# Kernel tuning notes

Hardware: AMD Instinct MI355X
Metric: run time of the kernel (lower is better)

The kernel has to match this reference:

```python
import jax, jax.numpy as jnp
import numpy as np

B, C, H, W = 8, 256, 128, 128
K = 7
DILS = (1, 2, 3)
HIDDEN = C // 16
EPS = 1e-5


def _bn(y, g, b, m, v):
    # eval-mode BatchNorm1d on (B,C,L)
    return (y - m[None, :, None]) * (g * jax.lax.rsqrt(v + EPS))[None, :, None] + b[None, :, None]


def _dw_conv1d(s, w, dil):
    # depthwise dilated Conv1d; s: (B,C,L), w: (C,1,K) torch layout == OIH
    pad = dil * (w.shape[-1] - 1) // 2
    return jax.lax.conv_general_dilated(
        s, w, window_strides=(1,), padding=[(pad, pad)],
        rhs_dilation=(dil,), dimension_numbers=('NCH', 'OIH', 'NCH'),
        feature_group_count=s.shape[1])


def _dir_weight(xp, sq_w, sq_b, convs, bn_g, bn_b, bn_m, bn_v):
    # xp: (B, L_ortho, C, L) -> weight (B, C, L)
    pmax = jnp.max(xp, axis=1)            # (B,C,L)
    pavg = jnp.mean(xp, axis=1)           # (B,C,L)
    # 1x1 Conv2d(2->1) == scalar mix of the two pooled maps
    s = sq_w[0] * pmax + sq_w[1] * pavg + sq_b
    y = _dw_conv1d(s, convs[0], DILS[0])
    for i in range(1, len(DILS)):
        y = y + _dw_conv1d(s, convs[i], DILS[i])
    return jax.nn.sigmoid(_bn(y, bn_g, bn_b, bn_m, bn_v))


def setup_inputs() -> dict:
    key = jax.random.key(0)
    ks = jax.random.split(key, 24)
    def n(k, shape, scale=0.1):
        return jax.random.normal(k, shape, dtype=jnp.float32) * scale
    return {
        "x": jax.random.normal(ks[0], (B, C, H, W), dtype=jnp.float32),
        "hw_sq_w": n(ks[1], (2,), 0.5), "hw_sq_b": n(ks[2], (1,), 0.1),
        "hw_conv": n(ks[3], (len(DILS), C, 1, K)),
        "hw_bn_g": 1.0 + n(ks[4], (C,)), "hw_bn_b": n(ks[5], (C,)),
        "hw_bn_m": n(ks[6], (C,)), "hw_bn_v": 1.0 + 0.1 * jax.random.uniform(ks[7], (C,)),
        "ww_sq_w": n(ks[8], (2,), 0.5), "ww_sq_b": n(ks[9], (1,), 0.1),
        "ww_conv": n(ks[10], (len(DILS), C, 1, K)),
        "ww_bn_g": 1.0 + n(ks[11], (C,)), "ww_bn_b": n(ks[12], (C,)),
        "ww_bn_m": n(ks[13], (C,)), "ww_bn_v": 1.0 + 0.1 * jax.random.uniform(ks[14], (C,)),
        "gate_w": 1.0 + n(ks[15], (C,)),
        "gate_bn_g": 1.0 + n(ks[16], (C,)), "gate_bn_b": n(ks[17], (C,)),
        "gate_bn_m": n(ks[18], (C,)), "gate_bn_v": 1.0 + 0.1 * jax.random.uniform(ks[19], (C,)),
        "mix_W": n(ks[20], (2, 2), 0.5), "mix_b": n(ks[21], (2,), 0.1),
        "ca_fc1": n(ks[22], (HIDDEN, C)), "ca_fc2": n(ks[23], (C, HIDDEN)),
        "alpha": jnp.float32(1.0), "beta": jnp.float32(1.0),
    }


def reference(x, hw_sq_w, hw_sq_b, hw_conv, hw_bn_g, hw_bn_b, hw_bn_m, hw_bn_v,
              ww_sq_w, ww_sq_b, ww_conv, ww_bn_g, ww_bn_b, ww_bn_m, ww_bn_v,
              gate_w, gate_bn_g, gate_bn_b, gate_bn_m, gate_bn_v,
              mix_W, mix_b, ca_fc1, ca_fc2, alpha, beta):
    b, c, h, w = x.shape
    # height-direction weight: pool over W, strip conv over H
    x_h_in = jnp.transpose(x, (0, 3, 1, 2))                                  # (B,W,C,H)
    w_h = _dir_weight(x_h_in, hw_sq_w, hw_sq_b, hw_conv, hw_bn_g, hw_bn_b, hw_bn_m, hw_bn_v)  # (B,C,H)
    x_h_out = jnp.transpose(x_h_in * w_h[:, None], (0, 2, 3, 1))             # (B,C,H,W)
    # width-direction weight: pool over H, strip conv over W
    x_w_in = jnp.transpose(x, (0, 2, 1, 3))                                  # (B,H,C,W)
    w_w = _dir_weight(x_w_in, ww_sq_w, ww_sq_b, ww_conv, ww_bn_g, ww_bn_b, ww_bn_m, ww_bn_v)  # (B,C,W)
    x_w_out = jnp.transpose(x_w_in * w_w[:, None], (0, 2, 1, 3))             # (B,C,H,W)

    # orientation mix (gate_fc is SHARED between directions)
    def gate(seq):  # (B,C,L) -> (B,C)
        y = jax.nn.relu(_bn(seq * gate_w[None, :, None], gate_bn_g, gate_bn_b, gate_bn_m, gate_bn_v))
        return jnp.mean(y, axis=-1)

    g = jnp.stack([gate(w_h), gate(w_w)], axis=-1)                           # (B,C,2)
    lam = jax.nn.softmax(g @ mix_W.T + mix_b, axis=-1)
    lam_h = lam[..., 0][:, :, None, None]
    lam_w = lam[..., 1][:, :, None, None]

    # channel attention (CBAM channel branch)
    xs = x.reshape(b, c, h * w)
    def fc(v):  # (B,C) -> (B,C)
        return jax.nn.relu(v @ ca_fc1.T) @ ca_fc2.T
    ca_w = jax.nn.sigmoid(fc(jnp.mean(xs, -1)) + fc(jnp.max(xs, -1)))[:, :, None, None]

    return x + alpha * (x_h_out * lam_h + x_w_out * lam_w) + beta * (x * ca_w)
```

## Files before the change

### kernel.cpp

```cpp
#include <hip/hip_runtime.h>

#define Bv 8
#define Cv 256
#define Hv 128
#define Wv 128
#define Kv 7
#define HID 16
#define EPS 1e-5f
#define BCn (Bv * Cv)
#define BCHn (BCn * Hv)

__device__ float g_wh[BCHn];
__device__ float g_ww[BCHn];
__device__ float g_gh[BCn];
__device__ float g_gw[BCn];
__device__ float g_mean[BCn];
__device__ float g_max[BCn];
__device__ float g_c0[BCn];
__device__ float g_cH[BCn];
__device__ float g_cW[BCn];

__global__ __launch_bounds__(256) void fused_pool_dir(
    const float* __restrict__ x,
    const float* __restrict__ hw_sq_w, const float* __restrict__ hw_sq_b,
    const float* __restrict__ hw_conv,
    const float* __restrict__ hw_bn_g, const float* __restrict__ hw_bn_b,
    const float* __restrict__ hw_bn_m, const float* __restrict__ hw_bn_v,
    const float* __restrict__ ww_sq_w, const float* __restrict__ ww_sq_b,
    const float* __restrict__ ww_conv,
    const float* __restrict__ ww_bn_g, const float* __restrict__ ww_bn_b,
    const float* __restrict__ ww_bn_m, const float* __restrict__ ww_bn_v,
    const float* __restrict__ gate_w,
    const float* __restrict__ gg, const float* __restrict__ gb,
    const float* __restrict__ gm, const float* __restrict__ gv)
{
    const int bc   = blockIdx.x;
    const int c    = bc & (Cv - 1);
    const size_t base = (size_t)bc * (Hv * Wv);
    const int tid  = threadIdx.x;
    const int lane = tid & 63;
    const int wv   = tid >> 6;
    const int half = lane >> 5;
    const int li   = lane & 31;
    const int w0   = li * 4;
    const int grp  = wv * 2 + half;

    __shared__ float ph_avg[Hv], ph_max[Hv];
    __shared__ float pw_avg[Wv], pw_max[Wv];
    __shared__ float lsum[8][Wv], lmax[8][Wv];
    __shared__ float sbuf[2][Hv];
    __shared__ float redS[4], redM[4];

    float cs0 = 0.f, cs1 = 0.f, cs2 = 0.f, cs3 = 0.f;
    float cm0 = -INFINITY, cm1 = -INFINITY, cm2 = -INFINITY, cm3 = -INFINITY;

    for (int j = 0; j < Hv / 8; ++j) {
        const int h = grp + 8 * j;
        const float4 u = *reinterpret_cast<const float4*>(x + base + (size_t)h * Wv + w0);
        const float a0 = u.x, a1 = u.y, a2 = u.z, a3 = u.w;
        cs0 += a0; cs1 += a1; cs2 += a2; cs3 += a3;
        cm0 = fmaxf(cm0, a0); cm1 = fmaxf(cm1, a1);
        cm2 = fmaxf(cm2, a2); cm3 = fmaxf(cm3, a3);
        float rs = (a0 + a1) + (a2 + a3);
        float rm = fmaxf(fmaxf(a0, a1), fmaxf(a2, a3));
        #pragma unroll
        for (int off = 16; off > 0; off >>= 1) {
            rs += __shfl_down(rs, off);
            rm = fmaxf(rm, __shfl_down(rm, off));
        }
        if (li == 0) { ph_avg[h] = rs * (1.0f / Wv); ph_max[h] = rm; }
    }
    lsum[grp][w0] = cs0; lsum[grp][w0+1] = cs1; lsum[grp][w0+2] = cs2; lsum[grp][w0+3] = cs3;
    lmax[grp][w0] = cm0; lmax[grp][w0+1] = cm1; lmax[grp][w0+2] = cm2; lmax[grp][w0+3] = cm3;
    __syncthreads();

    float s = 0.f, m = -INFINITY;
    if (tid < Wv) {
        #pragma unroll
        for (int g = 0; g < 8; ++g) { s += lsum[g][tid]; m = fmaxf(m, lmax[g][tid]); }
        pw_avg[tid] = s * (1.0f / Hv);
        pw_max[tid] = m;
    }
    #pragma unroll
    for (int off = 32; off > 0; off >>= 1) {
        s += __shfl_down(s, off);
        m = fmaxf(m, __shfl_down(m, off));
    }
    if (lane == 0) { redS[wv] = s; redM[wv] = m; }
    __syncthreads();
    if (tid == 0) {
        g_mean[bc] = (redS[0] + redS[1] + redS[2] + redS[3]) * (1.0f / (Hv * Wv));
        g_max[bc]  = fmaxf(fmaxf(redM[0], redM[1]), fmaxf(redM[2], redM[3]));
    }

    const int dir = tid >> 7;
    const int l   = tid & 127;
    const float* sqw = dir ? ww_sq_w : hw_sq_w;
    const float* sqb = dir ? ww_sq_b : hw_sq_b;
    const float pa = dir ? pw_avg[l] : ph_avg[l];
    const float pm = dir ? pw_max[l] : ph_max[l];
    sbuf[dir][l] = sqw[0] * pm + sqw[1] * pa + sqb[0];
    __syncthreads();

    const float* conv = dir ? ww_conv : hw_conv;
    float y = 0.f;
    #pragma unroll
    for (int d = 0; d < 3; ++d) {
        const int dil = d + 1;
        #pragma unroll
        for (int k = 0; k < Kv; ++k) {
            const int p = l + dil * (k - 3);
            const float sv = (p >= 0 && p < Hv) ? sbuf[dir][p] : 0.f;
            y += sv * conv[(d * Cv + c) * Kv + k];
        }
    }
    const float* bg = dir ? ww_bn_g : hw_bn_g;
    const float* bb = dir ? ww_bn_b : hw_bn_b;
    const float* bm = dir ? ww_bn_m : hw_bn_m;
    const float* bv = dir ? ww_bn_v : hw_bn_v;
    const float sc  = bg[c] * rsqrtf(bv[c] + EPS);
    const float yb  = (y - bm[c]) * sc + bb[c];
    const float wgt = 1.f / (1.f + expf(-yb));
    (dir ? g_ww : g_wh)[(size_t)bc * Hv + l] = wgt;

    const float gsc = gg[c] * rsqrtf(gv[c] + EPS);
    float gy = fmaxf((wgt * gate_w[c] - gm[c]) * gsc + gb[c], 0.f);
    #pragma unroll
    for (int off = 32; off > 0; off >>= 1) gy += __shfl_down(gy, off);
    if (lane == 0) redS[wv] = gy;
    __syncthreads();
    if (tid == 0) {
        g_gh[bc] = (redS[0] + redS[1]) * (1.0f / Hv);
        g_gw[bc] = (redS[2] + redS[3]) * (1.0f / Wv);
    }
}

__global__ __launch_bounds__(256) void mix_ca_kernel(
    const float* __restrict__ mix_W, const float* __restrict__ mix_b,
    const float* __restrict__ fc1,
    const float* __restrict__ fc2,
    const float* __restrict__ alpha_p, const float* __restrict__ beta_p)
{
    const int b = blockIdx.x;
    const int c = threadIdx.x;
    const int bc = b * Cv + c;
    __shared__ float vmean[Cv], vmax[Cv], hm[HID], hx[HID];

    vmean[c] = g_mean[bc];
    vmax[c]  = g_max[bc];
    __syncthreads();

    if (c < HID) {
        float am = 0.f, ax = 0.f;
        for (int j = 0; j < Cv; ++j) {
            const float f = fc1[c * Cv + j];
            am += vmean[j] * f;
            ax += vmax[j] * f;
        }
        hm[c] = fmaxf(am, 0.f);
        hx[c] = fmaxf(ax, 0.f);
    }
    __syncthreads();

    float om = 0.f, ox = 0.f;
    #pragma unroll
    for (int h = 0; h < HID; ++h) {
        const float f = fc2[c * HID + h];
        om += hm[h] * f;
        ox += hx[h] * f;
    }
    const float caw = 1.f / (1.f + expf(-(om + ox)));

    const float ghv = g_gh[bc], gwv = g_gw[bc];
    const float z0 = ghv * mix_W[0] + gwv * mix_W[1] + mix_b[0];
    const float z1 = ghv * mix_W[2] + gwv * mix_W[3] + mix_b[1];
    const float zm = fmaxf(z0, z1);
    const float e0 = expf(z0 - zm), e1 = expf(z1 - zm);
    const float inv = 1.f / (e0 + e1);

    const float alpha = alpha_p ? alpha_p[0] : 1.0f;
    const float beta  = beta_p  ? beta_p[0]  : 1.0f;
    g_c0[bc] = 1.f + beta * caw;
    g_cH[bc] = alpha * e0 * inv;
    g_cW[bc] = alpha * e1 * inv;
}

__global__ __launch_bounds__(256) void final_kernel(
    const float* __restrict__ x, float* __restrict__ out)
{
    const int bc = blockIdx.x;
    const size_t base = (size_t)bc * (Hv * Wv);
    const int tid  = threadIdx.x;
    const int lane = tid & 63;
    const int wv   = tid >> 6;
    const int half = lane >> 5;
    const int li   = lane & 31;
    const int w0   = li * 4;
    const int grp  = wv * 2 + half;

    __shared__ float cw[Wv];
    const float c0 = g_c0[bc];
    const float cH = g_cH[bc];
    if (tid < Wv) cw[tid] = g_cW[bc] * g_ww[(size_t)bc * Wv + tid];
    __syncthreads();

    const float cwa = cw[w0], cwb = cw[w0+1], cwc = cw[w0+2], cwd = cw[w0+3];

    for (int j = 0; j < Hv / 8; ++j) {
        const int h = grp + 8 * j;
        const float wh = c0 + cH * g_wh[(size_t)bc * Hv + h];
        const size_t off = base + (size_t)h * Wv + w0;
        const float4 u = *reinterpret_cast<const float4*>(x + off);
        float4 r;
        r.x = u.x * (wh + cwa);
        r.y = u.y * (wh + cwb);
        r.z = u.z * (wh + cwc);
        r.w = u.w * (wh + cwd);
        *reinterpret_cast<float4*>(out + off) = r;
    }
}

extern "C" void kernel_launch(void* const* d_in, const int* in_sizes, int n_in,
                              void* d_out, int out_size, void* d_ws, size_t ws_size,
                              hipStream_t stream)
{
    const float* x       = (const float*)d_in[0];
    const float* hw_sq_w = (const float*)d_in[1];
    const float* hw_sq_b = (const float*)d_in[2];
    const float* hw_conv = (const float*)d_in[3];
    const float* hw_bn_g = (const float*)d_in[4];
    const float* hw_bn_b = (const float*)d_in[5];
    const float* hw_bn_m = (const float*)d_in[6];
    const float* hw_bn_v = (const float*)d_in[7];
    const float* ww_sq_w = (const float*)d_in[8];
    const float* ww_sq_b = (const float*)d_in[9];
    const float* ww_conv = (const float*)d_in[10];
    const float* ww_bn_g = (const float*)d_in[11];
    const float* ww_bn_b = (const float*)d_in[12];
    const float* ww_bn_m = (const float*)d_in[13];
    const float* ww_bn_v = (const float*)d_in[14];
    const float* gate_w  = (const float*)d_in[15];
    const float* g_bn_g  = (const float*)d_in[16];
    const float* g_bn_b  = (const float*)d_in[17];
    const float* g_bn_m  = (const float*)d_in[18];
    const float* g_bn_v  = (const float*)d_in[19];
    const float* mix_W   = (const float*)d_in[20];
    const float* mix_b   = (const float*)d_in[21];
    const float* ca_fc1  = (const float*)d_in[22];
    const float* ca_fc2  = (const float*)d_in[23];
    const float* alpha_p = (n_in > 24) ? (const float*)d_in[24] : nullptr;
    const float* beta_p  = (n_in > 25) ? (const float*)d_in[25] : nullptr;
    float* out = (float*)d_out;
    (void)in_sizes; (void)out_size; (void)d_ws; (void)ws_size;

    fused_pool_dir<<<dim3(BCn), dim3(256), 0, stream>>>(
        x, hw_sq_w, hw_sq_b, hw_conv, hw_bn_g, hw_bn_b, hw_bn_m, hw_bn_v,
        ww_sq_w, ww_sq_b, ww_conv, ww_bn_g, ww_bn_b, ww_bn_m, ww_bn_v,
        gate_w, g_bn_g, g_bn_b, g_bn_m, g_bn_v);

    mix_ca_kernel<<<dim3(Bv), dim3(256), 0, stream>>>(
        mix_W, mix_b, ca_fc1, ca_fc2, alpha_p, beta_p);

    final_kernel<<<dim3(BCn), dim3(256), 0, stream>>>(x, out);
}
```

Before: 322.7 us.

## Fuse channel-attention/mix kernel into final kernel, use nontemporal stores and unrolling

Removes the small mix_ca kernel launch by recomputing the channel-attention MLP and orientation softmax per (b,c) block inside the final pass. The fc1 reduction is spread across all 256 threads with shuffles, and fc2, the mix softmax and the coefficients are computed by one thread per block. The output is written with nontemporal stores and the streaming loops are unrolled. This trades redundant MLP recomputation in 2048 blocks, plus three extra barriers, for one fewer launch and the removal of the global coefficient buffers.

```diff
diff --git a/kernel.cpp b/kernel.cpp
--- a/kernel.cpp
+++ b/kernel.cpp
@@ -10,15 +10,14 @@
 #define BCn (Bv * Cv)
 #define BCHn (BCn * Hv)
 
+typedef float vfloat4 __attribute__((ext_vector_type(4)));
+
 __device__ float g_wh[BCHn];
 __device__ float g_ww[BCHn];
 __device__ float g_gh[BCn];
 __device__ float g_gw[BCn];
 __device__ float g_mean[BCn];
 __device__ float g_max[BCn];
-__device__ float g_c0[BCn];
-__device__ float g_cH[BCn];
-__device__ float g_cW[BCn];
 
 __global__ __launch_bounds__(256) void fused_pool_dir(
     const float* __restrict__ x,
@@ -54,6 +53,7 @@
     float cs0 = 0.f, cs1 = 0.f, cs2 = 0.f, cs3 = 0.f;
     float cm0 = -INFINITY, cm1 = -INFINITY, cm2 = -INFINITY, cm3 = -INFINITY;
 
+    #pragma unroll 4
     for (int j = 0; j < Hv / 8; ++j) {
         const int h = grp + 8 * j;
         const float4 u = *reinterpret_cast<const float4*>(x + base + (size_t)h * Wv + w0);
@@ -135,60 +135,17 @@
     }
 }
 
-__global__ __launch_bounds__(256) void mix_ca_kernel(
+__global__ __launch_bounds__(256) void final_fused(
+    const float* __restrict__ x,
     const float* __restrict__ mix_W, const float* __restrict__ mix_b,
     const float* __restrict__ fc1,
     const float* __restrict__ fc2,
-    const float* __restrict__ alpha_p, const float* __restrict__ beta_p)
-{
-    const int b = blockIdx.x;
-    const int c = threadIdx.x;
-    const int bc = b * Cv + c;
-    __shared__ float vmean[Cv], vmax[Cv], hm[HID], hx[HID];
-
-    vmean[c] = g_mean[bc];
-    vmax[c]  = g_max[bc];
-    __syncthreads();
-
-    if (c < HID) {
-        float am = 0.f, ax = 0.f;
-        for (int j = 0; j < Cv; ++j) {
-            const float f = fc1[c * Cv + j];
-            am += vmean[j] * f;
-            ax += vmax[j] * f;
-        }
-        hm[c] = fmaxf(am, 0.f);
-        hx[c] = fmaxf(ax, 0.f);
-    }
-    __syncthreads();
-
-    float om = 0.f, ox = 0.f;
-    #pragma unroll
-    for (int h = 0; h < HID; ++h) {
-        const float f = fc2[c * HID + h];
-        om += hm[h] * f;
-        ox += hx[h] * f;
-    }
-    const float caw = 1.f / (1.f + expf(-(om + ox)));
-
-    const float ghv = g_gh[bc], gwv = g_gw[bc];
-    const float z0 = ghv * mix_W[0] + gwv * mix_W[1] + mix_b[0];
-    const float z1 = ghv * mix_W[2] + gwv * mix_W[3] + mix_b[1];
-    const float zm = fmaxf(z0, z1);
-    const float e0 = expf(z0 - zm), e1 = expf(z1 - zm);
-    const float inv = 1.f / (e0 + e1);
-
-    const float alpha = alpha_p ? alpha_p[0] : 1.0f;
-    const float beta  = beta_p  ? beta_p[0]  : 1.0f;
-    g_c0[bc] = 1.f + beta * caw;
-    g_cH[bc] = alpha * e0 * inv;
-    g_cW[bc] = alpha * e1 * inv;
-}
-
-__global__ __launch_bounds__(256) void final_kernel(
-    const float* __restrict__ x, float* __restrict__ out)
+    const float* __restrict__ alpha_p, const float* __restrict__ beta_p,
+    float* __restrict__ out)
 {
     const int bc = blockIdx.x;
+    const int b  = bc >> 8;
+    const int c  = bc & (Cv - 1);
     const size_t base = (size_t)bc * (Hv * Wv);
     const int tid  = threadIdx.x;
     const int lane = tid & 63;
@@ -198,25 +155,77 @@
     const int w0   = li * 4;
     const int grp  = wv * 2 + half;
 
+    __shared__ float vpool[2][Cv];
+    __shared__ float hmx[2][HID];
     __shared__ float cw[Wv];
-    const float c0 = g_c0[bc];
-    const float cH = g_cH[bc];
-    if (tid < Wv) cw[tid] = g_cW[bc] * g_ww[(size_t)bc * Wv + tid];
+    __shared__ float coef[3];
+
+    vpool[0][tid] = g_mean[b * Cv + tid];
+    vpool[1][tid] = g_max[b * Cv + tid];
+    __syncthreads();
+
+    {
+        const int which = tid >> 7;
+        const int j   = (tid & 127) >> 3;
+        const int sub = tid & 7;
+        const float* vs = vpool[which];
+        float part = 0.f;
+        #pragma unroll 8
+        for (int t = 0; t < 32; ++t) {
+            const int cc = sub * 32 + t;
+            part += vs[cc] * fc1[j * Cv + cc];
+        }
+        part += __shfl_down(part, 4);
+        part += __shfl_down(part, 2);
+        part += __shfl_down(part, 1);
+        if (sub == 0) hmx[which][j] = fmaxf(part, 0.f);
+    }
+    __syncthreads();
+
+    if (tid == 0) {
+        float om = 0.f, ox = 0.f;
+        #pragma unroll
+        for (int h = 0; h < HID; ++h) {
+            const float f = fc2[c * HID + h];
+            om += hmx[0][h] * f;
+            ox += hmx[1][h] * f;
+        }
+        const float caw = 1.f / (1.f + expf(-(om + ox)));
+
+        const float ghv = g_gh[bc], gwv = g_gw[bc];
+        const float z0 = ghv * mix_W[0] + gwv * mix_W[1] + mix_b[0];
+        const float z1 = ghv * mix_W[2] + gwv * mix_W[3] + mix_b[1];
+        const float zm = fmaxf(z0, z1);
+        const float e0 = expf(z0 - zm), e1 = expf(z1 - zm);
+        const float inv = 1.f / (e0 + e1);
+
+        const float alpha = alpha_p ? alpha_p[0] : 1.0f;
+        const float beta  = beta_p  ? beta_p[0]  : 1.0f;
+        coef[0] = 1.f + beta * caw;
+        coef[1] = alpha * e0 * inv;
+        coef[2] = alpha * e1 * inv;
+    }
+    __syncthreads();
+
+    const float c0 = coef[0];
+    const float cH = coef[1];
+    if (tid < Wv) cw[tid] = coef[2] * g_ww[(size_t)bc * Wv + tid];
     __syncthreads();
 
     const float cwa = cw[w0], cwb = cw[w0+1], cwc = cw[w0+2], cwd = cw[w0+3];
 
+    #pragma unroll 4
     for (int j = 0; j < Hv / 8; ++j) {
         const int h = grp + 8 * j;
         const float wh = c0 + cH * g_wh[(size_t)bc * Hv + h];
         const size_t off = base + (size_t)h * Wv + w0;
         const float4 u = *reinterpret_cast<const float4*>(x + off);
-        float4 r;
+        vfloat4 r;
         r.x = u.x * (wh + cwa);
         r.y = u.y * (wh + cwb);
         r.z = u.z * (wh + cwc);
         r.w = u.w * (wh + cwd);
-        *reinterpret_cast<float4*>(out + off) = r;
+        __builtin_nontemporal_store(r, reinterpret_cast<vfloat4*>(out + off));
     }
 }
 
@@ -258,8 +267,6 @@
         ww_sq_w, ww_sq_b, ww_conv, ww_bn_g, ww_bn_b, ww_bn_m, ww_bn_v,
         gate_w, g_bn_g, g_bn_b, g_bn_m, g_bn_v);
 
-    mix_ca_kernel<<<dim3(Bv), dim3(256), 0, stream>>>(
-        mix_W, mix_b, ca_fc1, ca_fc2, alpha_p, beta_p);
-
-    final_kernel<<<dim3(BCn), dim3(256), 0, stream>>>(x, out);
+    final_fused<<<dim3(BCn), dim3(256), 0, stream>>>(
+        x, mix_W, mix_b, ca_fc1, ca_fc2, alpha_p, beta_p, out);
 }
```

New measurement: 307.0 us. 4.9% less time.
